# Optimization experiments

Measured on AMD Instinct MI355X. Metric: run time of the kernel, lower is better.

Reference implementation:

```python
import jax, jax.numpy as jnp
import numpy as np

BETA = 0.9
THRESH = 1.0
SLOPE = 25.0  # fast_sigmoid surrogate slope

@jax.custom_vjp
def spike(x):
    # forward: heaviside(mem - threshold); backward: fast-sigmoid surrogate
    return (x > 0).astype(x.dtype)

def _spike_fwd(x):
    return (x > 0).astype(x.dtype), x

def _spike_bwd(x, g):
    return (g / (SLOPE * jnp.abs(x) + 1.0) ** 2,)

spike.defvjp(_spike_fwd, _spike_bwd)

def lif_step(mem, cur):
    # snntorch Leaky, reset_mechanism='subtract': reset from previous mem (detached)
    reset = jax.lax.stop_gradient((mem > THRESH).astype(cur.dtype))
    mem_new = BETA * mem + cur - reset * THRESH
    spk = spike(mem_new - THRESH)
    return spk, mem_new

def setup_inputs() -> dict:
    key = jax.random.key(0)
    ks = jax.random.split(key, 10)
    B, S, T = 256, 8, 25
    A, V, H, E = 512, 512, 256, 128
    a_seq = (jax.random.uniform(ks[0], (B, S, T, A)) < 0.2).astype(jnp.float32)
    v_seq = (jax.random.uniform(ks[1], (B, S, T, V)) < 0.2).astype(jnp.float32)
    def lin(kw, kb, out_d, in_d):
        lim = 1.0 / np.sqrt(in_d)
        W = jax.random.uniform(kw, (out_d, in_d), minval=-lim, maxval=lim, dtype=jnp.float32)
        b = jax.random.uniform(kb, (out_d,), minval=-lim, maxval=lim, dtype=jnp.float32)
        return W, b
    W_a1, b_a1 = lin(ks[2], ks[3], H, A)
    W_a2, b_a2 = lin(ks[4], ks[5], E, H)
    W_v1, b_v1 = lin(ks[6], ks[7], H, V)
    W_v2, b_v2 = lin(ks[8], ks[9], E, H)
    return dict(a_seq=a_seq, v_seq=v_seq, W_a1=W_a1, b_a1=b_a1, W_a2=W_a2, b_a2=b_a2,
                W_v1=W_v1, b_v1=b_v1, W_v2=W_v2, b_v2=b_v2)

def reference(a_seq, v_seq, W_a1, b_a1, W_a2, b_a2, W_v1, b_v1, W_v2, b_v2):
    B, S, T, A = a_seq.shape
    V = v_seq.shape[-1]
    H = W_a1.shape[0]
    E = W_a2.shape[0]
    BS = B * S  # segments are independent -> fold into batch
    a = a_seq.reshape(BS, T, A).transpose(1, 0, 2)  # [T, BS, A]
    v = v_seq.reshape(BS, T, V).transpose(1, 0, 2)  # [T, BS, V]

    def step(carry, xs):
        ma1, ma2, mv1, mv2, _, _ = carry
        at, vt = xs
        spk_a1, ma1 = lif_step(ma1, at @ W_a1.T + b_a1)
        spk_a2, ma2 = lif_step(ma2, spk_a1 @ W_a2.T + b_a2)
        spk_v1, mv1 = lif_step(mv1, vt @ W_v1.T + b_v1)
        spk_v2, mv2 = lif_step(mv2, spk_v1 @ W_v2.T + b_v2)
        return (ma1, ma2, mv1, mv2, spk_a2, spk_v2), None

    z = jnp.zeros
    init = (z((BS, H)), z((BS, E)), z((BS, H)), z((BS, E)), z((BS, E)), z((BS, E)))
    (ma1, ma2, mv1, mv2, spk_a2, spk_v2), _ = jax.lax.scan(step, init, (a, v))
    combined = jnp.concatenate([spk_a2, spk_v2], axis=1)  # [BS, 2E]
    norm = jnp.linalg.norm(combined, axis=1, keepdims=True)
    combined = combined / jnp.maximum(norm, 1e-12)  # F.normalize p=2 dim=1
    embs = combined.reshape(B, S, 2 * E)
    return embs.mean(axis=1)  # [B, 2E]
```

## Files before the change

kernel.cpp:

```cpp
#include <hip/hip_runtime.h>


typedef short bf16x8 __attribute__((ext_vector_type(8)));
typedef float f32x4 __attribute__((ext_vector_type(4)));

#define RBIG 51200

__global__ void prep_w(const float* __restrict__ Wa1, const float* __restrict__ Wv1,
                       const float* __restrict__ Wa2, const float* __restrict__ Wv2,
                       unsigned short* __restrict__ W1s, unsigned short* __restrict__ W2s) {
    int idx = blockIdx.x * 256 + threadIdx.x;
    float w;
    unsigned short* dst;
    int K, k;
    if (idx < 262144) {
        int p = idx >> 17, rem = idx & 131071;
        int n = rem >> 9; k = rem & 511; K = 512;
        const float* src = p ? Wv1 : Wa1;
        w = src[(size_t)n * 512 + k];
        dst = W1s + (size_t)p * 256 * 1536 + (size_t)n * 1536;
    } else {
        int j = idx - 262144;
        int p = j >> 15, rem = j & 32767;
        int n = rem >> 8; k = rem & 255; K = 256;
        const float* src = p ? Wv2 : Wa2;
        w = src[(size_t)n * 256 + k];
        dst = W2s + (size_t)p * 128 * 768 + (size_t)n * 768;
    }
    unsigned int u  = __float_as_uint(w);
    unsigned int hi = u & 0xFFFF0000u;
    float r1 = w - __uint_as_float(hi);
    unsigned int mi = __float_as_uint(r1) & 0xFFFF0000u;
    float r2 = r1 - __uint_as_float(mi);
    dst[k]         = (unsigned short)(hi >> 16);
    dst[K + k]     = (unsigned short)(mi >> 16);
    dst[2 * K + k] = (unsigned short)(__float_as_uint(r2) >> 16);
}

template <int KSRC, int NT, bool AF32>
__global__ __launch_bounds__(256, 2) void gemm_spl(
    const void* __restrict__ A0, const void* __restrict__ A1,
    const unsigned short* __restrict__ Ws, float* __restrict__ C) {
    constexpr int KE  = 3 * KSRC;
    constexpr int NKB = KSRC / 64;
    constexpr int NC  = 3 * NKB;

    __shared__ unsigned short As[2][128 * 64];
    __shared__ unsigned short Bs[2][128 * 64];

    const int tid  = threadIdx.x;
    const int bx   = blockIdx.x, by = blockIdx.y, bz = blockIdx.z;
    const int lane = tid & 63, wave = tid >> 6;
    const int wm   = wave >> 1, wn = wave & 1;
    const size_t row0 = (size_t)bx * 128;
    const unsigned short* Wp = Ws + (size_t)bz * NT * KE + (size_t)by * 128 * KE;

    f32x4 acc[4][4];
    f32x4 zz = {0.f, 0.f, 0.f, 0.f};
#pragma unroll
    for (int i = 0; i < 4; ++i)
#pragma unroll
        for (int j = 0; j < 4; ++j) acc[i][j] = zz;

    auto stageA = [&](int buf, int kb) {
        if constexpr (AF32) {
            const float* Ag = (const float*)(bz ? A1 : A0);
#pragma unroll
            for (int j = 0; j < 8; ++j) {
                int lin = tid + (j << 8);
                int row = lin >> 4, f4 = lin & 15;
                float4 v = *(const float4*)(Ag + (row0 + row) * KSRC + kb * 64 + (f4 << 2));
                uint2 pk;
                pk.x = (__float_as_uint(v.y) & 0xFFFF0000u) | (__float_as_uint(v.x) >> 16);
                pk.y = (__float_as_uint(v.w) & 0xFFFF0000u) | (__float_as_uint(v.z) >> 16);
                int idx = (row * 64 + (f4 << 2)) ^ ((row & 7) << 3);
                *(uint2*)&As[buf][idx] = pk;
            }
        } else {
            const unsigned short* Ag = (const unsigned short*)(bz ? A1 : A0);
#pragma unroll
            for (int j = 0; j < 4; ++j) {
                int slot = (tid << 3) + (j << 11);
                int row = slot >> 6, col = slot & 63;
                uint4 v = *(const uint4*)(Ag + (row0 + row) * KSRC + kb * 64 + col);
                int idx = slot ^ ((row & 7) << 3);
                *(uint4*)&As[buf][idx] = v;
            }
        }
    };
    auto stageB = [&](int buf, int kb, int s) {
        const unsigned short* Bg = Wp + (size_t)s * KSRC + kb * 64;
#pragma unroll
        for (int j = 0; j < 4; ++j) {
            int slot = (tid << 3) + (j << 11);
            int row = slot >> 6, col = slot & 63;
            uint4 v = *(const uint4*)(Bg + (size_t)row * KE + col);
            int idx = slot ^ ((row & 7) << 3);
            *(uint4*)&Bs[buf][idx] = v;
        }
    };

    stageA(0, 0);
    stageB(0, 0, 0);
    int kb = 0, s = 0;
    const int swz = (lane & 7) << 3;
    for (int c = 0; c < NC; ++c) {
        __syncthreads();
        int s1 = s + 1, kb1 = kb;
        if (s1 == 3) { s1 = 0; kb1 = kb + 1; }
        if (c + 1 < NC) {
            stageB((c + 1) & 1, kb1, s1);
            if (s1 == 0) stageA(kb1 & 1, kb1);
        }
        const unsigned short* Ab = As[kb & 1];
        const unsigned short* Bb = Bs[c & 1];
#pragma unroll
        for (int ks = 0; ks < 2; ++ks) {
            int ko = ks * 32 + ((lane >> 4) << 3);
            bf16x8 af[4], bb[4];
#pragma unroll
            for (int mi2 = 0; mi2 < 4; ++mi2) {
                int Rm = wm * 64 + mi2 * 16 + (lane & 15);
                af[mi2] = *(const bf16x8*)&Ab[(Rm * 64 + ko) ^ swz];
            }
#pragma unroll
            for (int ni = 0; ni < 4; ++ni) {
                int Rn = wn * 64 + ni * 16 + (lane & 15);
                bb[ni] = *(const bf16x8*)&Bb[(Rn * 64 + ko) ^ swz];
            }
#pragma unroll
            for (int mi2 = 0; mi2 < 4; ++mi2)
#pragma unroll
                for (int ni = 0; ni < 4; ++ni)
                    acc[mi2][ni] = __builtin_amdgcn_mfma_f32_16x16x32_bf16(
                        af[mi2], bb[ni], acc[mi2][ni], 0, 0, 0);
        }
        kb = kb1; s = s1;
    }

    float* Cp = C + (size_t)bz * RBIG * NT;
    int r4 = ((lane >> 4) << 2), cl = lane & 15;
#pragma unroll
    for (int mi2 = 0; mi2 < 4; ++mi2)
#pragma unroll
        for (int ni = 0; ni < 4; ++ni) {
            size_t col = (size_t)by * 128 + wn * 64 + ni * 16 + cl;
#pragma unroll
            for (int j = 0; j < 4; ++j) {
                size_t row = row0 + wm * 64 + mi2 * 16 + r4 + j;
                Cp[row * NT + col] = acc[mi2][ni][j];
            }
        }
}

__global__ void lif1_k(const float* __restrict__ cur, const float* __restrict__ ba1,
                       const float* __restrict__ bv1, unsigned int* __restrict__ spk) {
    int r = blockIdx.x, p = blockIdx.y, d = threadIdx.x;
    const float* c0 = cur + ((size_t)p * RBIG + (size_t)r * 25) * 256 + 2 * d;
    const float* bias = p ? bv1 : ba1;
    float b0 = bias[2 * d], b1 = bias[2 * d + 1];
    float2 cv[25];
#pragma unroll
    for (int t = 0; t < 25; ++t) cv[t] = *(const float2*)(c0 + (size_t)t * 256);
    unsigned int* sp = spk + ((size_t)p * RBIG + (size_t)r * 25) * 128 + d;
    float m0 = 0.f, m1 = 0.f;
#pragma unroll
    for (int t = 0; t < 25; ++t) {
        float r0 = (m0 > 1.f) ? 1.f : 0.f;
        float r1 = (m1 > 1.f) ? 1.f : 0.f;
        m0 = 0.9f * m0 + (cv[t].x + b0) - r0;
        m1 = 0.9f * m1 + (cv[t].y + b1) - r1;
        unsigned int w = (m0 > 1.f ? 0x3F80u : 0u) | (m1 > 1.f ? 0x3F800000u : 0u);
        sp[(size_t)t * 128] = w;
    }
}

__global__ void lif2_k(const float* __restrict__ cur2, const float* __restrict__ ba2,
                       const float* __restrict__ bv2, float* __restrict__ spk2) {
    int r = blockIdx.x, p = blockIdx.y, d = threadIdx.x;
    const float* c0 = cur2 + ((size_t)p * RBIG + (size_t)r * 25) * 128 + 2 * d;
    const float* bias = p ? bv2 : ba2;
    float b0 = bias[2 * d], b1 = bias[2 * d + 1];
    float2 cv[25];
#pragma unroll
    for (int t = 0; t < 25; ++t) cv[t] = *(const float2*)(c0 + (size_t)t * 128);
    float m0 = 0.f, m1 = 0.f;
#pragma unroll
    for (int t = 0; t < 25; ++t) {
        float r0 = (m0 > 1.f) ? 1.f : 0.f;
        float r1 = (m1 > 1.f) ? 1.f : 0.f;
        m0 = 0.9f * m0 + (cv[t].x + b0) - r0;
        m1 = 0.9f * m1 + (cv[t].y + b1) - r1;
    }
    float2 o;
    o.x = (m0 > 1.f) ? 1.f : 0.f;
    o.y = (m1 > 1.f) ? 1.f : 0.f;
    *(float2*)(spk2 + ((size_t)p * 2048 + r) * 128 + 2 * d) = o;
}

__global__ void epi_k(const float* __restrict__ spk2, float* __restrict__ out) {
    int b = blockIdx.x, d = threadIdx.x;
    int p = d >> 7, e = d & 127;
    __shared__ float part[4];
    float acc = 0.f;
    for (int s = 0; s < 8; ++s) {
        float v = spk2[((size_t)p * 2048 + (size_t)(b * 8 + s)) * 128 + e];
        float sq = v;
#pragma unroll
        for (int off = 32; off > 0; off >>= 1) sq += __shfl_down(sq, off);
        if ((d & 63) == 0) part[d >> 6] = sq;
        __syncthreads();
        float nrm = sqrtf(part[0] + part[1] + part[2] + part[3]);
        acc += v / fmaxf(nrm, 1e-12f);
        __syncthreads();
    }
    out[(size_t)b * 256 + d] = acc * 0.125f;
}

extern "C" void kernel_launch(void* const* d_in, const int* in_sizes, int n_in,
                              void* d_out, int out_size, void* d_ws, size_t ws_size,
                              hipStream_t stream) {
    const float* a_seq = (const float*)d_in[0];
    const float* v_seq = (const float*)d_in[1];
    const float* W_a1  = (const float*)d_in[2];
    const float* b_a1  = (const float*)d_in[3];
    const float* W_a2  = (const float*)d_in[4];
    const float* b_a2  = (const float*)d_in[5];
    const float* W_v1  = (const float*)d_in[6];
    const float* b_v1  = (const float*)d_in[7];
    const float* W_v2  = (const float*)d_in[8];
    const float* b_v2  = (const float*)d_in[9];

    char* ws = (char*)d_ws;
    unsigned short* W1s  = (unsigned short*)(ws);
    unsigned short* W2s  = (unsigned short*)(ws + 1572864);
    unsigned short* spk1 = (unsigned short*)(ws + 1966080);
    float*          curb = (float*)(ws + 54394880);
    float*          spk2 = (float*)(ws + 159252480);
    float*          out  = (float*)d_out;

    prep_w<<<1280, 256, 0, stream>>>(W_a1, W_v1, W_a2, W_v2, W1s, W2s);

    gemm_spl<512, 256, true><<<dim3(400, 2, 2), 256, 0, stream>>>(a_seq, v_seq, W1s, curb);
    lif1_k<<<dim3(2048, 2), 128, 0, stream>>>(curb, b_a1, b_v1, (unsigned int*)spk1);

    gemm_spl<256, 128, false><<<dim3(400, 1, 2), 256, 0, stream>>>(
        spk1, spk1 + (size_t)RBIG * 256, W2s, curb);
    lif2_k<<<dim3(2048, 2), 64, 0, stream>>>(curb, b_a2, b_v2, spk2);

    epi_k<<<256, 256, 0, stream>>>(spk2, out);
}
```

Baseline: 377.2 us.

## Enlarge GEMM tiles to 256 rows with 8 waves and register-staged prefetch

Replaces the 128x128, 4-wave split-bf16 GEMM with a 512-thread kernel using 256-row tiles that cover the full N width per block. Global loads for the next K chunk are issued into registers before the MFMA phase and written to LDS afterward, with one barrier per iteration. MFMA issue is wrapped in s_setprio. This aims to cut redundant A reloads across N tiles and to hide global latency, at the cost of more registers and LDS, which may reduce occupancy.

```diff
diff --git a/kernel.cpp b/kernel.cpp
--- a/kernel.cpp
+++ b/kernel.cpp
@@ -37,118 +37,192 @@
     dst[2 * K + k] = (unsigned short)(__float_as_uint(r2) >> 16);
 }
 
-template <int KSRC, int NT, bool AF32>
-__global__ __launch_bounds__(256, 2) void gemm_spl(
+template <int KSRC, int NT, int WM, int WN, bool AF32>
+__global__ __launch_bounds__(512, 2) void gemm8(
     const void* __restrict__ A0, const void* __restrict__ A1,
     const unsigned short* __restrict__ Ws, float* __restrict__ C) {
+    constexpr int BM  = 256, BN = NT;
     constexpr int KE  = 3 * KSRC;
     constexpr int NKB = KSRC / 64;
     constexpr int NC  = 3 * NKB;
-
-    __shared__ unsigned short As[2][128 * 64];
-    __shared__ unsigned short Bs[2][128 * 64];
+    constexpr int MFR = BM / WM / 16;
+    constexpr int NFR = BN / WN / 16;
+    constexpr int NPH = MFR / 2;
+    constexpr int NBB = BN * 64 / 8 / 512;
+
+    __shared__ unsigned short As[2][BM * 64];
+    __shared__ unsigned short Bs[2][BN * 64];
 
     const int tid  = threadIdx.x;
-    const int bx   = blockIdx.x, by = blockIdx.y, bz = blockIdx.z;
+    const int bx   = blockIdx.x, bz = blockIdx.y;
     const int lane = tid & 63, wave = tid >> 6;
-    const int wm   = wave >> 1, wn = wave & 1;
-    const size_t row0 = (size_t)bx * 128;
-    const unsigned short* Wp = Ws + (size_t)bz * NT * KE + (size_t)by * 128 * KE;
-
-    f32x4 acc[4][4];
+    const int wm   = wave / WN, wn = wave % WN;
+    const size_t row0 = (size_t)bx * BM;
+    const unsigned short* Wp = Ws + (size_t)bz * NT * KE;
+
+    f32x4 acc[MFR][NFR];
     f32x4 zz = {0.f, 0.f, 0.f, 0.f};
 #pragma unroll
-    for (int i = 0; i < 4; ++i)
-#pragma unroll
-        for (int j = 0; j < 4; ++j) acc[i][j] = zz;
-
-    auto stageA = [&](int buf, int kb) {
+    for (int i = 0; i < MFR; ++i)
+#pragma unroll
+        for (int j = 0; j < NFR; ++j) acc[i][j] = zz;
+
+    auto loadB = [&](int kb, int s, uint4 (&r)[NBB]) {
+        const unsigned short* Bg = Wp + (size_t)s * KSRC + (size_t)kb * 64;
+#pragma unroll
+        for (int j = 0; j < NBB; ++j) {
+            int slot = tid + j * 512;
+            int row = slot >> 3, c8 = (slot & 7) << 3;
+            r[j] = *(const uint4*)(Bg + (size_t)row * KE + c8);
+        }
+    };
+    auto writeB = [&](int buf, uint4 (&r)[NBB]) {
+#pragma unroll
+        for (int j = 0; j < NBB; ++j) {
+            int slot = tid + j * 512;
+            int row = slot >> 3, c8 = (slot & 7) << 3;
+            int idx = (row * 64 + c8) ^ ((row & 7) << 3);
+            *(uint4*)&Bs[buf][idx] = r[j];
+        }
+    };
+    auto loadAf = [&](int kb, float4 (&r)[8]) {
+        const float* Ag = (const float*)(bz ? A1 : A0);
+#pragma unroll
+        for (int j = 0; j < 4; ++j) {
+            int pi = tid + j * 512;
+            int row = pi >> 3, c = (pi & 7) << 3;
+            const float* p = Ag + (row0 + row) * KSRC + kb * 64 + c;
+            r[2 * j]     = *(const float4*)(p);
+            r[2 * j + 1] = *(const float4*)(p + 4);
+        }
+    };
+    auto writeAf = [&](int buf, float4 (&r)[8]) {
+#pragma unroll
+        for (int j = 0; j < 4; ++j) {
+            int pi = tid + j * 512;
+            int row = pi >> 3, c = (pi & 7) << 3;
+            float4 v0 = r[2 * j], v1 = r[2 * j + 1];
+            uint4 u;
+            u.x = (__float_as_uint(v0.y) & 0xFFFF0000u) | (__float_as_uint(v0.x) >> 16);
+            u.y = (__float_as_uint(v0.w) & 0xFFFF0000u) | (__float_as_uint(v0.z) >> 16);
+            u.z = (__float_as_uint(v1.y) & 0xFFFF0000u) | (__float_as_uint(v1.x) >> 16);
+            u.w = (__float_as_uint(v1.w) & 0xFFFF0000u) | (__float_as_uint(v1.z) >> 16);
+            int idx = (row * 64 + c) ^ ((row & 7) << 3);
+            *(uint4*)&As[buf][idx] = u;
+        }
+    };
+    auto loadAu = [&](int kb, uint4 (&r)[4]) {
+        const unsigned short* Ag = (const unsigned short*)(bz ? A1 : A0);
+#pragma unroll
+        for (int j = 0; j < 4; ++j) {
+            int slot = tid + j * 512;
+            int row = slot >> 3, c8 = (slot & 7) << 3;
+            r[j] = *(const uint4*)(Ag + (row0 + row) * KSRC + kb * 64 + c8);
+        }
+    };
+    auto writeAu = [&](int buf, uint4 (&r)[4]) {
+#pragma unroll
+        for (int j = 0; j < 4; ++j) {
+            int slot = tid + j * 512;
+            int row = slot >> 3, c8 = (slot & 7) << 3;
+            int idx = (row * 64 + c8) ^ ((row & 7) << 3);
+            *(uint4*)&As[buf][idx] = r[j];
+        }
+    };
+
+    {
+        uint4 bR[NBB];
+        loadB(0, 0, bR);
         if constexpr (AF32) {
-            const float* Ag = (const float*)(bz ? A1 : A0);
-#pragma unroll
-            for (int j = 0; j < 8; ++j) {
-                int lin = tid + (j << 8);
-                int row = lin >> 4, f4 = lin & 15;
-                float4 v = *(const float4*)(Ag + (row0 + row) * KSRC + kb * 64 + (f4 << 2));
-                uint2 pk;
-                pk.x = (__float_as_uint(v.y) & 0xFFFF0000u) | (__float_as_uint(v.x) >> 16);
-                pk.y = (__float_as_uint(v.w) & 0xFFFF0000u) | (__float_as_uint(v.z) >> 16);
-                int idx = (row * 64 + (f4 << 2)) ^ ((row & 7) << 3);
-                *(uint2*)&As[buf][idx] = pk;
+            float4 aR[8];
+            loadAf(0, aR);
+            writeAf(0, aR);
+        } else {
+            uint4 aR[4];
+            loadAu(0, aR);
+            writeAu(0, aR);
+        }
+        writeB(0, bR);
+    }
+    __syncthreads();
+
+    const int swz = (lane & 7) << 3;
+    const int ko0 = (lane >> 4) << 3;
+    const int rfr = lane & 15;
+
+    int kb = 0, s = 0;
+    for (int c = 0; c < NC; ++c) {
+        int s1 = (s == 2) ? 0 : s + 1;
+        int kb1 = (s1 == 0) ? kb + 1 : kb;
+        const bool haveNext = (c + 1 < NC);
+
+        uint4 bR[NBB];
+        float4 aRf[8];
+        uint4 aRu[4];
+        if (haveNext) {
+            loadB(kb1, s1, bR);
+            if (s1 == 0) {
+                if constexpr (AF32) loadAf(kb1, aRf);
+                else                loadAu(kb1, aRu);
             }
-        } else {
-            const unsigned short* Ag = (const unsigned short*)(bz ? A1 : A0);
-#pragma unroll
-            for (int j = 0; j < 4; ++j) {
-                int slot = (tid << 3) + (j << 11);
-                int row = slot >> 6, col = slot & 63;
-                uint4 v = *(const uint4*)(Ag + (row0 + row) * KSRC + kb * 64 + col);
-                int idx = slot ^ ((row & 7) << 3);
-                *(uint4*)&As[buf][idx] = v;
-            }
-        }
-    };
-    auto stageB = [&](int buf, int kb, int s) {
-        const unsigned short* Bg = Wp + (size_t)s * KSRC + kb * 64;
-#pragma unroll
-        for (int j = 0; j < 4; ++j) {
-            int slot = (tid << 3) + (j << 11);
-            int row = slot >> 6, col = slot & 63;
-            uint4 v = *(const uint4*)(Bg + (size_t)row * KE + col);
-            int idx = slot ^ ((row & 7) << 3);
-            *(uint4*)&Bs[buf][idx] = v;
-        }
-    };
-
-    stageA(0, 0);
-    stageB(0, 0, 0);
-    int kb = 0, s = 0;
-    const int swz = (lane & 7) << 3;
-    for (int c = 0; c < NC; ++c) {
-        __syncthreads();
-        int s1 = s + 1, kb1 = kb;
-        if (s1 == 3) { s1 = 0; kb1 = kb + 1; }
-        if (c + 1 < NC) {
-            stageB((c + 1) & 1, kb1, s1);
-            if (s1 == 0) stageA(kb1 & 1, kb1);
-        }
+        }
+
         const unsigned short* Ab = As[kb & 1];
         const unsigned short* Bb = Bs[c & 1];
-#pragma unroll
-        for (int ks = 0; ks < 2; ++ks) {
-            int ko = ks * 32 + ((lane >> 4) << 3);
-            bf16x8 af[4], bb[4];
-#pragma unroll
-            for (int mi2 = 0; mi2 < 4; ++mi2) {
-                int Rm = wm * 64 + mi2 * 16 + (lane & 15);
-                af[mi2] = *(const bf16x8*)&Ab[(Rm * 64 + ko) ^ swz];
+        bf16x8 bb[NFR][2];
+#pragma unroll
+        for (int ph = 0; ph < NPH; ++ph) {
+            if (ph == 0) {
+#pragma unroll
+                for (int ni = 0; ni < NFR; ++ni)
+#pragma unroll
+                    for (int ks = 0; ks < 2; ++ks) {
+                        int Rn = wn * (BN / WN) + ni * 16 + rfr;
+                        bb[ni][ks] = *(const bf16x8*)&Bb[(Rn * 64 + ks * 32 + ko0) ^ swz];
+                    }
             }
-#pragma unroll
-            for (int ni = 0; ni < 4; ++ni) {
-                int Rn = wn * 64 + ni * 16 + (lane & 15);
-                bb[ni] = *(const bf16x8*)&Bb[(Rn * 64 + ko) ^ swz];
+            bf16x8 af[2][2];
+#pragma unroll
+            for (int q = 0; q < 2; ++q)
+#pragma unroll
+                for (int ks = 0; ks < 2; ++ks) {
+                    int Rm = wm * (BM / WM) + (2 * ph + q) * 16 + rfr;
+                    af[q][ks] = *(const bf16x8*)&Ab[(Rm * 64 + ks * 32 + ko0) ^ swz];
+                }
+            __builtin_amdgcn_s_setprio(1);
+#pragma unroll
+            for (int q = 0; q < 2; ++q)
+#pragma unroll
+                for (int ni = 0; ni < NFR; ++ni)
+#pragma unroll
+                    for (int ks = 0; ks < 2; ++ks)
+                        acc[2 * ph + q][ni] = __builtin_amdgcn_mfma_f32_16x16x32_bf16(
+                            af[q][ks], bb[ni][ks], acc[2 * ph + q][ni], 0, 0, 0);
+            __builtin_amdgcn_s_setprio(0);
+        }
+
+        if (haveNext) {
+            if (s1 == 0) {
+                if constexpr (AF32) writeAf(kb1 & 1, aRf);
+                else                writeAu(kb1 & 1, aRu);
             }
-#pragma unroll
-            for (int mi2 = 0; mi2 < 4; ++mi2)
-#pragma unroll
-                for (int ni = 0; ni < 4; ++ni)
-                    acc[mi2][ni] = __builtin_amdgcn_mfma_f32_16x16x32_bf16(
-                        af[mi2], bb[ni], acc[mi2][ni], 0, 0, 0);
-        }
+            writeB((c + 1) & 1, bR);
+        }
+        __syncthreads();
         kb = kb1; s = s1;
     }
 
     float* Cp = C + (size_t)bz * RBIG * NT;
     int r4 = ((lane >> 4) << 2), cl = lane & 15;
 #pragma unroll
-    for (int mi2 = 0; mi2 < 4; ++mi2)
-#pragma unroll
-        for (int ni = 0; ni < 4; ++ni) {
-            size_t col = (size_t)by * 128 + wn * 64 + ni * 16 + cl;
+    for (int mi = 0; mi < MFR; ++mi)
+#pragma unroll
+        for (int ni = 0; ni < NFR; ++ni) {
+            size_t col = (size_t)wn * (BN / WN) + ni * 16 + cl;
 #pragma unroll
             for (int j = 0; j < 4; ++j) {
-                size_t row = row0 + wm * 64 + mi2 * 16 + r4 + j;
-                Cp[row * NT + col] = acc[mi2][ni][j];
+                size_t row = row0 + wm * (BM / WM) + mi * 16 + r4 + j;
+                Cp[row * NT + col] = acc[mi][ni][j];
             }
         }
 }
@@ -241,10 +315,10 @@
 
     prep_w<<<1280, 256, 0, stream>>>(W_a1, W_v1, W_a2, W_v2, W1s, W2s);
 
-    gemm_spl<512, 256, true><<<dim3(400, 2, 2), 256, 0, stream>>>(a_seq, v_seq, W1s, curb);
+    gemm8<512, 256, 2, 4, true><<<dim3(200, 2), 512, 0, stream>>>(a_seq, v_seq, W1s, curb);
     lif1_k<<<dim3(2048, 2), 128, 0, stream>>>(curb, b_a1, b_v1, (unsigned int*)spk1);
 
-    gemm_spl<256, 128, false><<<dim3(400, 1, 2), 256, 0, stream>>>(
+    gemm8<256, 128, 4, 2, false><<<dim3(200, 2), 512, 0, stream>>>(
         spk1, spk1 + (size_t)RBIG * 256, W2s, curb);
     lif2_k<<<dim3(2048, 2), 64, 0, stream>>>(curb, b_a2, b_v2, spk2);
 
```

Result: slower. 473.7 us (+25.6%).

## Use direct global-to-LDS loads in templated GEMM and fuse LIF2 with epilogue

Applied to the files above, without the earlier changes.

The GEMM kernel is rewritten as a templated kernel that stages A and B tiles with global_load_lds (direct global-to-LDS transfers), so registers are no longer used for staging. For fp32 A inputs the bf16 truncation now happens when fragments are read from LDS rather than at stage time. Tile shapes change: layer 1 covers the full N=256 per block with 512 threads, and layer 2 uses 64-row tiles with more blocks. The second LIF step and the normalize/mean epilogue are merged into a single tail kernel, which removes the spk2 buffer and one launch. The tail kernel has only 256 blocks running the sequential LIF, and fp32 A tiles now take twice the LDS space.

```diff
diff --git a/kernel.cpp b/kernel.cpp
--- a/kernel.cpp
+++ b/kernel.cpp
@@ -5,6 +5,11 @@
 typedef float f32x4 __attribute__((ext_vector_type(4)));
 
 #define RBIG 51200
+
+__device__ __forceinline__ void glds16(const void* g, void* l) {
+    __builtin_amdgcn_global_load_lds((const __attribute__((address_space(1))) void*)g,
+                                     (__attribute__((address_space(3))) void*)l, 16, 0, 0);
+}
 
 __global__ void prep_w(const float* __restrict__ Wa1, const float* __restrict__ Wv1,
                        const float* __restrict__ Wa2, const float* __restrict__ Wv2,
@@ -37,118 +42,136 @@
     dst[2 * K + k] = (unsigned short)(__float_as_uint(r2) >> 16);
 }
 
-template <int KSRC, int NT, bool AF32>
-__global__ __launch_bounds__(256, 2) void gemm_spl(
+template <int KSRC, int NT, int BM, int BN, int NTHR, int WMW, int WNW, int MINW, bool AF32>
+__global__ __launch_bounds__(NTHR, MINW) void gemmG(
     const void* __restrict__ A0, const void* __restrict__ A1,
     const unsigned short* __restrict__ Ws, float* __restrict__ C) {
-    constexpr int KE  = 3 * KSRC;
-    constexpr int NKB = KSRC / 64;
-    constexpr int NC  = 3 * NKB;
-
-    __shared__ unsigned short As[2][128 * 64];
-    __shared__ unsigned short Bs[2][128 * 64];
-
-    const int tid  = threadIdx.x;
-    const int bx   = blockIdx.x, by = blockIdx.y, bz = blockIdx.z;
-    const int lane = tid & 63, wave = tid >> 6;
-    const int wm   = wave >> 1, wn = wave & 1;
-    const size_t row0 = (size_t)bx * 128;
-    const unsigned short* Wp = Ws + (size_t)bz * NT * KE + (size_t)by * 128 * KE;
-
-    f32x4 acc[4][4];
+    constexpr int KE     = 3 * KSRC;
+    constexpr int NC     = 3 * (KSRC / 64);
+    constexpr int MFR    = BM / WMW / 16;
+    constexpr int NFR    = BN / WNW / 16;
+    constexpr int AESZ   = AF32 ? 4 : 2;
+    constexpr int ABYTES = BM * 64 * AESZ;
+    constexpr int BBYTES = BN * 64 * 2;
+    constexpr int NAG    = ABYTES / 16 / NTHR;
+    constexpr int NBG    = BBYTES / 16 / NTHR;
+
+    __shared__ __align__(1024) char lds[2 * ABYTES + 2 * BBYTES];
+
+    const int tid  = threadIdx.x, lane = tid & 63, wave = tid >> 6;
+    const int wm   = wave / WNW, wn = wave % WNW;
+    const int bx   = blockIdx.x, bz = blockIdx.z;
+    const size_t row0 = (size_t)bx * BM;
+
+    const char* Abase = (const char*)(bz ? A1 : A0) + row0 * KSRC * AESZ;
+    const char* Bbase = (const char*)Ws + (size_t)bz * NT * KE * 2;
+
+    size_t offA[NAG];
+    int dA[NAG];
+#pragma unroll
+    for (int j = 0; j < NAG; ++j) {
+        int G = tid + j * NTHR;
+        int row, sl;
+        if constexpr (AF32) { row = G >> 4; sl = G & 15; }
+        else                { row = G >> 3; sl = G & 7; }
+        offA[j] = (size_t)row * KSRC * AESZ + (size_t)((sl ^ (row & 7)) << 4);
+        dA[j]   = wave * 1024 + j * NTHR * 16;
+    }
+    size_t offB[NBG];
+    int dB[NBG];
+#pragma unroll
+    for (int j = 0; j < NBG; ++j) {
+        int G = tid + j * NTHR;
+        int n = G >> 3, sl = G & 7;
+        offB[j] = (size_t)n * KE * 2 + (size_t)((sl ^ (n & 7)) << 4);
+        dB[j]   = wave * 1024 + j * NTHR * 16;
+    }
+
+    auto stageA = [&](int kb) {
+        const char* s = Abase + (size_t)kb * 64 * AESZ;
+        char* d = lds + (kb & 1) * ABYTES;
+#pragma unroll
+        for (int j = 0; j < NAG; ++j) glds16(s + offA[j], d + dA[j]);
+    };
+    auto stageB = [&](int kb, int sh, int buf) {
+        const char* s = Bbase + ((size_t)sh * KSRC + (size_t)kb * 64) * 2;
+        char* d = lds + 2 * ABYTES + buf * BBYTES;
+#pragma unroll
+        for (int j = 0; j < NBG; ++j) glds16(s + offB[j], d + dB[j]);
+    };
+
+    f32x4 acc[MFR][NFR];
     f32x4 zz = {0.f, 0.f, 0.f, 0.f};
 #pragma unroll
-    for (int i = 0; i < 4; ++i)
-#pragma unroll
-        for (int j = 0; j < 4; ++j) acc[i][j] = zz;
-
-    auto stageA = [&](int buf, int kb) {
-        if constexpr (AF32) {
-            const float* Ag = (const float*)(bz ? A1 : A0);
-#pragma unroll
-            for (int j = 0; j < 8; ++j) {
-                int lin = tid + (j << 8);
-                int row = lin >> 4, f4 = lin & 15;
-                float4 v = *(const float4*)(Ag + (row0 + row) * KSRC + kb * 64 + (f4 << 2));
-                uint2 pk;
-                pk.x = (__float_as_uint(v.y) & 0xFFFF0000u) | (__float_as_uint(v.x) >> 16);
-                pk.y = (__float_as_uint(v.w) & 0xFFFF0000u) | (__float_as_uint(v.z) >> 16);
-                int idx = (row * 64 + (f4 << 2)) ^ ((row & 7) << 3);
-                *(uint2*)&As[buf][idx] = pk;
+    for (int i = 0; i < MFR; ++i)
+#pragma unroll
+        for (int j = 0; j < NFR; ++j) acc[i][j] = zz;
+
+    stageA(0);
+    stageB(0, 0, 0);
+    __syncthreads();
+
+    const int rfr = lane & 15;
+    int kb = 0, s = 0;
+    for (int c = 0; c < NC; ++c) {
+        int s1 = (s == 2) ? 0 : s + 1;
+        int kb1 = (s1 == 0) ? kb + 1 : kb;
+        if (c + 1 < NC) {
+            stageB(kb1, s1, (c + 1) & 1);
+            if (s1 == 0) stageA(kb1);
+        }
+
+        const char* Ab = lds + (kb & 1) * ABYTES;
+        const unsigned short* Bb = (const unsigned short*)(lds + 2 * ABYTES + (c & 1) * BBYTES);
+#pragma unroll
+        for (int ks = 0; ks < 2; ++ks) {
+            const int kbase = ks * 32 + ((lane >> 4) << 3);
+            bf16x8 bb[NFR];
+#pragma unroll
+            for (int ni = 0; ni < NFR; ++ni) {
+                int n = wn * (BN / WNW) + ni * 16 + rfr;
+                bb[ni] = *(const bf16x8*)&Bb[(n * 64 + kbase) ^ ((n & 7) << 3)];
             }
-        } else {
-            const unsigned short* Ag = (const unsigned short*)(bz ? A1 : A0);
-#pragma unroll
-            for (int j = 0; j < 4; ++j) {
-                int slot = (tid << 3) + (j << 11);
-                int row = slot >> 6, col = slot & 63;
-                uint4 v = *(const uint4*)(Ag + (row0 + row) * KSRC + kb * 64 + col);
-                int idx = slot ^ ((row & 7) << 3);
-                *(uint4*)&As[buf][idx] = v;
+#pragma unroll
+            for (int mi = 0; mi < MFR; ++mi) {
+                int r = wm * (BM / WMW) + mi * 16 + rfr;
+                bf16x8 av;
+                if constexpr (AF32) {
+                    const float* Af = (const float*)Ab;
+                    int e1 = (r * 64 + kbase) ^ ((r & 7) << 2);
+                    uint4 ua = *(const uint4*)&Af[e1];
+                    uint4 ub = *(const uint4*)&Af[e1 ^ 4];
+                    uint4 w;
+                    w.x = (ua.y & 0xFFFF0000u) | (ua.x >> 16);
+                    w.y = (ua.w & 0xFFFF0000u) | (ua.z >> 16);
+                    w.z = (ub.y & 0xFFFF0000u) | (ub.x >> 16);
+                    w.w = (ub.w & 0xFFFF0000u) | (ub.z >> 16);
+                    av = __builtin_bit_cast(bf16x8, w);
+                } else {
+                    const unsigned short* Au = (const unsigned short*)Ab;
+                    av = *(const bf16x8*)&Au[(r * 64 + kbase) ^ ((r & 7) << 3)];
+                }
+#pragma unroll
+                for (int ni = 0; ni < NFR; ++ni)
+                    acc[mi][ni] = __builtin_amdgcn_mfma_f32_16x16x32_bf16(
+                        av, bb[ni], acc[mi][ni], 0, 0, 0);
             }
         }
-    };
-    auto stageB = [&](int buf, int kb, int s) {
-        const unsigned short* Bg = Wp + (size_t)s * KSRC + kb * 64;
-#pragma unroll
-        for (int j = 0; j < 4; ++j) {
-            int slot = (tid << 3) + (j << 11);
-            int row = slot >> 6, col = slot & 63;
-            uint4 v = *(const uint4*)(Bg + (size_t)row * KE + col);
-            int idx = slot ^ ((row & 7) << 3);
-            *(uint4*)&Bs[buf][idx] = v;
-        }
-    };
-
-    stageA(0, 0);
-    stageB(0, 0, 0);
-    int kb = 0, s = 0;
-    const int swz = (lane & 7) << 3;
-    for (int c = 0; c < NC; ++c) {
         __syncthreads();
-        int s1 = s + 1, kb1 = kb;
-        if (s1 == 3) { s1 = 0; kb1 = kb + 1; }
-        if (c + 1 < NC) {
-            stageB((c + 1) & 1, kb1, s1);
-            if (s1 == 0) stageA(kb1 & 1, kb1);
-        }
-        const unsigned short* Ab = As[kb & 1];
-        const unsigned short* Bb = Bs[c & 1];
-#pragma unroll
-        for (int ks = 0; ks < 2; ++ks) {
-            int ko = ks * 32 + ((lane >> 4) << 3);
-            bf16x8 af[4], bb[4];
-#pragma unroll
-            for (int mi2 = 0; mi2 < 4; ++mi2) {
-                int Rm = wm * 64 + mi2 * 16 + (lane & 15);
-                af[mi2] = *(const bf16x8*)&Ab[(Rm * 64 + ko) ^ swz];
-            }
-#pragma unroll
-            for (int ni = 0; ni < 4; ++ni) {
-                int Rn = wn * 64 + ni * 16 + (lane & 15);
-                bb[ni] = *(const bf16x8*)&Bb[(Rn * 64 + ko) ^ swz];
-            }
-#pragma unroll
-            for (int mi2 = 0; mi2 < 4; ++mi2)
-#pragma unroll
-                for (int ni = 0; ni < 4; ++ni)
-                    acc[mi2][ni] = __builtin_amdgcn_mfma_f32_16x16x32_bf16(
-                        af[mi2], bb[ni], acc[mi2][ni], 0, 0, 0);
-        }
         kb = kb1; s = s1;
     }
 
     float* Cp = C + (size_t)bz * RBIG * NT;
     int r4 = ((lane >> 4) << 2), cl = lane & 15;
 #pragma unroll
-    for (int mi2 = 0; mi2 < 4; ++mi2)
-#pragma unroll
-        for (int ni = 0; ni < 4; ++ni) {
-            size_t col = (size_t)by * 128 + wn * 64 + ni * 16 + cl;
+    for (int mi = 0; mi < MFR; ++mi)
+#pragma unroll
+        for (int ni = 0; ni < NFR; ++ni) {
+            size_t col = (size_t)wn * (BN / WNW) + ni * 16 + cl;
 #pragma unroll
             for (int j = 0; j < 4; ++j) {
-                size_t row = row0 + wm * 64 + mi2 * 16 + r4 + j;
-                Cp[row * NT + col] = acc[mi2][ni][j];
+                size_t row = row0 + wm * (BM / WMW) + mi * 16 + r4 + j;
+                Cp[row * NT + col] = acc[mi][ni][j];
             }
         }
 }
@@ -175,36 +198,27 @@
     }
 }
 
-__global__ void lif2_k(const float* __restrict__ cur2, const float* __restrict__ ba2,
-                       const float* __restrict__ bv2, float* __restrict__ spk2) {
-    int r = blockIdx.x, p = blockIdx.y, d = threadIdx.x;
-    const float* c0 = cur2 + ((size_t)p * RBIG + (size_t)r * 25) * 128 + 2 * d;
-    const float* bias = p ? bv2 : ba2;
-    float b0 = bias[2 * d], b1 = bias[2 * d + 1];
-    float2 cv[25];
-#pragma unroll
-    for (int t = 0; t < 25; ++t) cv[t] = *(const float2*)(c0 + (size_t)t * 128);
-    float m0 = 0.f, m1 = 0.f;
-#pragma unroll
-    for (int t = 0; t < 25; ++t) {
-        float r0 = (m0 > 1.f) ? 1.f : 0.f;
-        float r1 = (m1 > 1.f) ? 1.f : 0.f;
-        m0 = 0.9f * m0 + (cv[t].x + b0) - r0;
-        m1 = 0.9f * m1 + (cv[t].y + b1) - r1;
-    }
-    float2 o;
-    o.x = (m0 > 1.f) ? 1.f : 0.f;
-    o.y = (m1 > 1.f) ? 1.f : 0.f;
-    *(float2*)(spk2 + ((size_t)p * 2048 + r) * 128 + 2 * d) = o;
-}
-
-__global__ void epi_k(const float* __restrict__ spk2, float* __restrict__ out) {
+__global__ void tail_k(const float* __restrict__ cur2, const float* __restrict__ ba2,
+                       const float* __restrict__ bv2, float* __restrict__ out) {
     int b = blockIdx.x, d = threadIdx.x;
     int p = d >> 7, e = d & 127;
+    const float* bias = p ? bv2 : ba2;
+    float bo = bias[e];
     __shared__ float part[4];
     float acc = 0.f;
     for (int s = 0; s < 8; ++s) {
-        float v = spk2[((size_t)p * 2048 + (size_t)(b * 8 + s)) * 128 + e];
+        int r = b * 8 + s;
+        const float* c0 = cur2 + ((size_t)p * RBIG + (size_t)r * 25) * 128 + e;
+        float cv[25];
+#pragma unroll
+        for (int t = 0; t < 25; ++t) cv[t] = c0[(size_t)t * 128];
+        float m = 0.f;
+#pragma unroll
+        for (int t = 0; t < 25; ++t) {
+            float rs = (m > 1.f) ? 1.f : 0.f;
+            m = 0.9f * m + (cv[t] + bo) - rs;
+        }
+        float v = (m > 1.f) ? 1.f : 0.f;
         float sq = v;
 #pragma unroll
         for (int off = 32; off > 0; off >>= 1) sq += __shfl_down(sq, off);
@@ -236,17 +250,17 @@
     unsigned short* W2s  = (unsigned short*)(ws + 1572864);
     unsigned short* spk1 = (unsigned short*)(ws + 1966080);
     float*          curb = (float*)(ws + 54394880);
-    float*          spk2 = (float*)(ws + 159252480);
     float*          out  = (float*)d_out;
 
     prep_w<<<1280, 256, 0, stream>>>(W_a1, W_v1, W_a2, W_v2, W1s, W2s);
 
-    gemm_spl<512, 256, true><<<dim3(400, 2, 2), 256, 0, stream>>>(a_seq, v_seq, W1s, curb);
+    gemmG<512, 256, 128, 256, 512, 2, 4, 2, true>
+        <<<dim3(400, 1, 2), 512, 0, stream>>>(a_seq, v_seq, W1s, curb);
     lif1_k<<<dim3(2048, 2), 128, 0, stream>>>(curb, b_a1, b_v1, (unsigned int*)spk1);
 
-    gemm_spl<256, 128, false><<<dim3(400, 1, 2), 256, 0, stream>>>(
+    gemmG<256, 128, 64, 128, 256, 2, 2, 3, false>
+        <<<dim3(800, 1, 2), 256, 0, stream>>>(
         spk1, spk1 + (size_t)RBIG * 256, W2s, curb);
-    lif2_k<<<dim3(2048, 2), 64, 0, stream>>>(curb, b_a2, b_v2, spk2);
-
-    epi_k<<<256, 256, 0, stream>>>(spk2, out);
-}
+
+    tail_k<<<256, 256, 0, stream>>>(curb, b_a2, b_v2, out);
+}
```

Result: slower. 421.8 us (+11.8%).
